# Kernel optimization log

Measured on AMD Instinct MI355X. Metric: run time of the kernel, lower is better.

Reference implementation:

```python
import jax, jax.numpy as jnp
import numpy as np

B, N, C, NH = 4, 2304, 256, 8
HD = C // NH            # head dim = 32
HS = WS = 48            # H = W = sqrt(N)
RADIUS = 3.0
MLP_HID = 4 * C
SCALE = HD ** (-0.5)
NEG = -1e9              # stands in for -inf (identical softmax up to fp eps)
EPS = 1e-6


def spatial_mask():
    # get_spatial_mask: cdist of (y, x) grid coords, -inf where dist > radius
    yy, xx = jnp.meshgrid(jnp.arange(HS), jnp.arange(WS), indexing='ij')
    coords = jnp.stack([yy, xx], -1).reshape(-1, 2).astype(jnp.float32)  # [N, 2]
    d2 = jnp.sum((coords[:, None, :] - coords[None, :, :]) ** 2, -1)     # [N, N]
    return jnp.where(d2 > RADIUS * RADIUS, NEG, 0.0)


def layernorm(x, g, b):
    mu = jnp.mean(x, -1, keepdims=True)
    var = jnp.mean((x - mu) ** 2, -1, keepdims=True)
    return (x - mu) * jax.lax.rsqrt(var + EPS) * g + b


def setup_inputs() -> dict:
    key = jax.random.key(0)
    ks = jax.random.split(key, 16)
    s = 0.02
    return {
        'x':    jax.random.normal(ks[0], (B, N, C), jnp.float32),
        'x_kv': jax.random.normal(ks[1], (B, N, C), jnp.float32),
        'Wq': jax.random.normal(ks[2], (C, C), jnp.float32) * s,
        'bq': jnp.zeros((C,), jnp.float32),
        'Wk': jax.random.normal(ks[3], (C, C), jnp.float32) * s,
        'bk': jnp.zeros((C,), jnp.float32),
        'Wv': jax.random.normal(ks[4], (C, C), jnp.float32) * s,
        'bv': jnp.zeros((C,), jnp.float32),
        'Wp': jax.random.normal(ks[5], (C, C), jnp.float32) * s,
        'bp': jnp.zeros((C,), jnp.float32),
        'g1': jnp.ones((C,), jnp.float32),
        'b1': jnp.zeros((C,), jnp.float32),
        'g2': jnp.ones((C,), jnp.float32),
        'b2': jnp.zeros((C,), jnp.float32),
        'W1': jax.random.normal(ks[6], (C, MLP_HID), jnp.float32) * s,
        'bm1': jnp.zeros((MLP_HID,), jnp.float32),
        'W2': jax.random.normal(ks[7], (MLP_HID, C), jnp.float32) * s,
        'bm2': jnp.zeros((C,), jnp.float32),
    }


def reference(x, x_kv, Wq, bq, Wk, bk, Wv, bv, Wp, bp,
              g1, b1, g2, b2, W1, bm1, W2, bm2):
    mask = spatial_mask()                                  # [N, N]
    h = layernorm(x, g1, b1)
    hkv = layernorm(x_kv, g1, b1)
    q = (h @ Wq + bq).reshape(B, N, NH, HD)
    k = (hkv @ Wk + bk).reshape(B, N, NH, HD)
    v = (hkv @ Wv + bv).reshape(B, N, NH, HD)
    scores = jnp.einsum('bqhd,bkhd->bhqk', q, k) * SCALE + mask
    attn = jax.nn.softmax(scores, axis=-1)
    out = jnp.einsum('bhqk,bkhd->bqhd', attn, v).reshape(B, N, C)
    x = x + out @ Wp + bp
    m = layernorm(x, g2, b2)
    x = x + jax.nn.gelu(m @ W1 + bm1, approximate=False) @ W2 + bm2
    return x
```

## Files before the change

kernel.cpp:

```cpp
#include <hip/hip_runtime.h>
#include <hip/hip_fp16.h>
#include <math.h>

#define BB 4
#define NN 2304
#define CC 256
#define HS 48
#define HID 1024
#define BNROWS (BB * NN)
#define ATTN_SCALE 0.17677669529663687f

typedef _Float16 f16;
typedef __attribute__((ext_vector_type(2))) _Float16 h2;
typedef __attribute__((ext_vector_type(8))) _Float16 h8;
typedef __attribute__((ext_vector_type(4))) float f4;

static __device__ __forceinline__ float wave_sum64(float v) {
    v += __shfl_xor(v, 32, 64);
    v += __shfl_xor(v, 16, 64);
    v += __shfl_xor(v, 8, 64);
    v += __shfl_xor(v, 4, 64);
    v += __shfl_xor(v, 2, 64);
    v += __shfl_xor(v, 1, 64);
    return v;
}

__global__ __launch_bounds__(256) void prep_kernel(
    const float* __restrict__ Wq, const float* __restrict__ Wk,
    const float* __restrict__ Wv, const float* __restrict__ Wp,
    const float* __restrict__ W1, const float* __restrict__ W2,
    const float* __restrict__ bq, const float* __restrict__ bk,
    const float* __restrict__ bv,
    f16* __restrict__ WqkvT, f16* __restrict__ WpT,
    f16* __restrict__ W1T, f16* __restrict__ W2T, float* __restrict__ bqkv)
{
    int bx = blockIdx.x;
    if (bx == 768) {
        const int t = threadIdx.x;
        bqkv[t]       = bq[t];
        bqkv[t + 256] = bk[t];
        bqkv[t + 512] = bv[t];
        return;
    }
    __shared__ float tt[32][33];
    const float* src; f16* dst; int K, N;
    if (bx < 64)        { src = Wq; dst = WqkvT;             K = 256;  N = 256; }
    else if (bx < 128)  { src = Wk; dst = WqkvT + 65536;     K = 256;  N = 256;  bx -= 64; }
    else if (bx < 192)  { src = Wv; dst = WqkvT + 131072;    K = 256;  N = 256;  bx -= 128; }
    else if (bx < 256)  { src = Wp; dst = WpT;               K = 256;  N = 256;  bx -= 192; }
    else if (bx < 512)  { src = W1; dst = W1T;               K = 256;  N = 1024; bx -= 256; }
    else                { src = W2; dst = W2T;               K = 1024; N = 256;  bx -= 512; }
    const int tN = N >> 5;
    const int kt = bx / tN, nt = bx - kt * tN;
    const int rr = threadIdx.x >> 5, cc = threadIdx.x & 31;
#pragma unroll
    for (int j = 0; j < 4; ++j)
        tt[rr + 8 * j][cc] = src[(size_t)(kt * 32 + rr + 8 * j) * N + nt * 32 + cc];
    __syncthreads();
#pragma unroll
    for (int j = 0; j < 4; ++j)
        dst[(size_t)(nt * 32 + rr + 8 * j) * K + kt * 32 + cc] = (f16)tt[cc][rr + 8 * j];
}

__global__ __launch_bounds__(256) void ln1_kernel(
    const float* __restrict__ x, const float* __restrict__ xkv,
    const float* __restrict__ g, const float* __restrict__ be,
    f16* __restrict__ hq, f16* __restrict__ hkv)
{
    const int r = blockIdx.x * 4 + (threadIdx.x >> 6);
    const int lane = threadIdx.x & 63;
    const float* src; f16* dst;
    if (r < BNROWS) { src = x + (size_t)r * CC;             dst = hq + (size_t)r * CC; }
    else { src = xkv + (size_t)(r - BNROWS) * CC; dst = hkv + (size_t)(r - BNROWS) * CC; }
    const float4 v = ((const float4*)src)[lane];
    const float mu = wave_sum64(v.x + v.y + v.z + v.w) * (1.0f / CC);
    const float d0 = v.x - mu, d1 = v.y - mu, d2 = v.z - mu, d3 = v.w - mu;
    const float var = wave_sum64(d0 * d0 + d1 * d1 + d2 * d2 + d3 * d3) * (1.0f / CC);
    const float rs = rsqrtf(var + 1e-6f);
    const float4 g4 = ((const float4*)g)[lane];
    const float4 b4 = ((const float4*)be)[lane];
    h2 o01 = (h2){(f16)(d0 * rs * g4.x + b4.x), (f16)(d1 * rs * g4.y + b4.y)};
    h2 o23 = (h2){(f16)(d2 * rs * g4.z + b4.z), (f16)(d3 * rs * g4.w + b4.w)};
    ((h2*)dst)[lane * 2] = o01;
    ((h2*)dst)[lane * 2 + 1] = o23;
}

__global__ __launch_bounds__(256) void ln2_kernel(
    const f16* __restrict__ x1, const float* __restrict__ g,
    const float* __restrict__ be, f16* __restrict__ m2)
{
    const int r = blockIdx.x * 4 + (threadIdx.x >> 6);
    const int lane = threadIdx.x & 63;
    const f16* src = x1 + (size_t)r * CC;
    const h2 a01 = ((const h2*)src)[lane * 2];
    const h2 a23 = ((const h2*)src)[lane * 2 + 1];
    const float v0 = (float)a01[0], v1 = (float)a01[1];
    const float v2 = (float)a23[0], v3 = (float)a23[1];
    const float mu = wave_sum64(v0 + v1 + v2 + v3) * (1.0f / CC);
    const float d0 = v0 - mu, d1 = v1 - mu, d2 = v2 - mu, d3 = v3 - mu;
    const float var = wave_sum64(d0 * d0 + d1 * d1 + d2 * d2 + d3 * d3) * (1.0f / CC);
    const float rs = rsqrtf(var + 1e-6f);
    const float4 g4 = ((const float4*)g)[lane];
    const float4 b4 = ((const float4*)be)[lane];
    f16* dst = m2 + (size_t)r * CC;
    h2 o01 = (h2){(f16)(d0 * rs * g4.x + b4.x), (f16)(d1 * rs * g4.y + b4.y)};
    h2 o23 = (h2){(f16)(d2 * rs * g4.z + b4.z), (f16)(d3 * rs * g4.w + b4.w)};
    ((h2*)dst)[lane * 2] = o01;
    ((h2*)dst)[lane * 2 + 1] = o23;
}

template <bool GELU, int RESID, bool OUTF32, bool QKV>
__global__ __launch_bounds__(256) void gemm64(
    const f16* __restrict__ Aq, const f16* __restrict__ Akv,
    const f16* __restrict__ Bt, const float* __restrict__ bias,
    const void* __restrict__ resid, void* __restrict__ out1,
    void* __restrict__ outkv, int M, int N, int K)
{
    __shared__ f16 As[64][72];
    __shared__ f16 Bs[64][72];
    const int tid = threadIdx.x;
    const int wid = tid >> 6, lane = tid & 63;
    const int ln15 = lane & 15, quad = lane >> 4;
    const int m0 = blockIdx.y * 64;
    const int n0 = blockIdx.x * 64;
    const bool kv = QKV && (n0 >= 256);
    const f16* Ap = (QKV && kv) ? Akv : Aq;

    const int sr = tid >> 2;
    const int sk = (tid & 3) << 4;

    f4 acc[4];
#pragma unroll
    for (int i = 0; i < 4; ++i) acc[i] = (f4){0.f, 0.f, 0.f, 0.f};

    for (int k0 = 0; k0 < K; k0 += 64) {
        const f16* ag = Ap + (size_t)(m0 + sr) * K + k0 + sk;
        const f16* bg = Bt + (size_t)(n0 + sr) * K + k0 + sk;
        *(uint4*)&As[sr][sk]     = *(const uint4*)ag;
        *(uint4*)&As[sr][sk + 8] = *(const uint4*)(ag + 8);
        *(uint4*)&Bs[sr][sk]     = *(const uint4*)bg;
        *(uint4*)&Bs[sr][sk + 8] = *(const uint4*)(bg + 8);
        __syncthreads();
#pragma unroll
        for (int kh = 0; kh < 2; ++kh) {
            const h8 bF = *(const h8*)&Bs[wid * 16 + ln15][kh * 32 + quad * 8];
#pragma unroll
            for (int mt = 0; mt < 4; ++mt) {
                const h8 aF = *(const h8*)&As[mt * 16 + ln15][kh * 32 + quad * 8];
                acc[mt] = __builtin_amdgcn_mfma_f32_16x16x32_f16(aF, bF, acc[mt], 0, 0, 0);
            }
        }
        __syncthreads();
    }

    const int gn = n0 + wid * 16 + ln15;
    const float bs = bias[gn];
#pragma unroll
    for (int mt = 0; mt < 4; ++mt) {
#pragma unroll
        for (int r = 0; r < 4; ++r) {
            const int gm = m0 + mt * 16 + quad * 4 + r;
            float v = acc[mt][r] + bs;
            if (GELU) v = 0.5f * v * (1.0f + erff(v * 0.70710678118654752f));
            if (RESID == 1) v += ((const float*)resid)[(size_t)gm * N + gn];
            if (RESID == 2) v += (float)((const f16*)resid)[(size_t)gm * N + gn];
            if (QKV) {
                if (kv) ((f16*)outkv)[(size_t)gm * 512 + (gn - 256)] = (f16)v;
                else    ((f16*)out1)[(size_t)gm * 256 + gn] = (f16)v;
            } else if (OUTF32) {
                ((float*)out1)[(size_t)gm * N + gn] = v;
            } else {
                ((f16*)out1)[(size_t)gm * N + gn] = (f16)v;
            }
        }
    }
}

__device__ __constant__ int ATT_DY[29] = {
    -3, -2, -2, -2, -2, -2, -1, -1, -1, -1, -1, 0, 0, 0, 0,
    0, 0, 0, 1, 1, 1, 1, 1, 2, 2, 2, 2, 2, 3};
__device__ __constant__ int ATT_DX[29] = {
    0, -2, -1, 0, 1, 2, -2, -1, 0, 1, 2, -3, -2, -1, 0,
    1, 2, 3, -2, -1, 0, 1, 2, -2, -1, 0, 1, 2, 0};

__global__ __launch_bounds__(128) void attn_tile_kernel(
    const f16* __restrict__ qf, const f16* __restrict__ kvf,
    f16* __restrict__ ao)
{
    __shared__ f16 ks[196][66];
    __shared__ f16 vs[196][66];
    const int tile = blockIdx.x, hp = blockIdx.y, b = blockIdx.z;
    const int ty0 = (tile / 6) * 8, tx0 = (tile - (tile / 6) * 6) * 8;
    const int tid = threadIdx.x;

    for (int idx = tid; idx < 196 * 16; idx += 128) {
        const int r = idx >> 4, seg = idx & 15;
        const int gy = ty0 - 3 + r / 14, gx = tx0 - 3 + (r - (r / 14) * 14);
        uint4 val = {0u, 0u, 0u, 0u};
        if ((unsigned)gy < HS && (unsigned)gx < HS) {
            const size_t rowb = ((size_t)b * NN + gy * HS + gx) * 512;
            const int ch = (seg < 8) ? (hp * 64 + seg * 8)
                                     : (256 + hp * 64 + (seg - 8) * 8);
            val = *(const uint4*)&kvf[rowb + ch];
        }
        f16* dstp = (seg < 8) ? &ks[r][(seg & 7) * 8] : &vs[r][(seg & 7) * 8];
        ((unsigned int*)dstp)[0] = val.x;
        ((unsigned int*)dstp)[1] = val.y;
        ((unsigned int*)dstp)[2] = val.z;
        ((unsigned int*)dstp)[3] = val.w;
    }
    __syncthreads();

    const int q = tid & 63, hh = tid >> 6;
    const int qy = q >> 3, qx = q & 7;
    const size_t qrow = (size_t)b * NN + (ty0 + qy) * HS + tx0 + qx;
    const f16* qp = qf + qrow * CC + hp * 64 + hh * 32;
    uint4 qa[4];
#pragma unroll
    for (int i = 0; i < 4; ++i) qa[i] = ((const uint4*)qp)[i];
    const h2* q2 = (const h2*)qa;

    float s[29];
#pragma unroll
    for (int n = 0; n < 29; ++n) {
        const int dy = ATT_DY[n], dx = ATT_DX[n];
        const int r = (qy + 3 + dy) * 14 + qx + 3 + dx;
        const bool valid = (unsigned)(ty0 + qy + dy) < HS &&
                           (unsigned)(tx0 + qx + dx) < HS;
        float a = 0.0f;
        const h2* kp = (const h2*)&ks[r][hh * 32];
#pragma unroll
        for (int i = 0; i < 16; ++i)
            a = __builtin_amdgcn_fdot2(q2[i], kp[i], a, false);
        s[n] = valid ? a * ATTN_SCALE : -1e30f;
    }
    float m = s[0];
#pragma unroll
    for (int n = 1; n < 29; ++n) m = fmaxf(m, s[n]);
    float l = 0.0f;
#pragma unroll
    for (int n = 0; n < 29; ++n) { s[n] = __expf(s[n] - m); l += s[n]; }
    h2 a2[16];
#pragma unroll
    for (int i = 0; i < 16; ++i) a2[i] = (h2){(f16)0.f, (f16)0.f};
#pragma unroll
    for (int n = 0; n < 29; ++n) {
        const int dy = ATT_DY[n], dx = ATT_DX[n];
        const int r = (qy + 3 + dy) * 14 + qx + 3 + dx;
        const f16 pn = (f16)s[n];
        const h2 ph = (h2){pn, pn};
        const h2* vp = (const h2*)&vs[r][hh * 32];
#pragma unroll
        for (int i = 0; i < 16; ++i) a2[i] += ph * vp[i];
    }
    const float inv = 1.0f / l;
    uint4 ov[4];
    f16* oh = (f16*)ov;
#pragma unroll
    for (int i = 0; i < 16; ++i) {
        oh[2 * i]     = (f16)((float)a2[i][0] * inv);
        oh[2 * i + 1] = (f16)((float)a2[i][1] * inv);
    }
    uint4* dst = (uint4*)(ao + qrow * CC + hp * 64 + hh * 32);
#pragma unroll
    for (int i = 0; i < 4; ++i) dst[i] = ov[i];
}

extern "C" void kernel_launch(void* const* d_in, const int* in_sizes, int n_in,
                              void* d_out, int out_size, void* d_ws, size_t ws_size,
                              hipStream_t stream) {
    const float* x    = (const float*)d_in[0];
    const float* x_kv = (const float*)d_in[1];
    const float* Wq   = (const float*)d_in[2];
    const float* bq   = (const float*)d_in[3];
    const float* Wk   = (const float*)d_in[4];
    const float* bk   = (const float*)d_in[5];
    const float* Wv   = (const float*)d_in[6];
    const float* bv   = (const float*)d_in[7];
    const float* Wp   = (const float*)d_in[8];
    const float* bp   = (const float*)d_in[9];
    const float* g1   = (const float*)d_in[10];
    const float* b1   = (const float*)d_in[11];
    const float* g2   = (const float*)d_in[12];
    const float* b2   = (const float*)d_in[13];
    const float* W1   = (const float*)d_in[14];
    const float* bm1  = (const float*)d_in[15];
    const float* W2   = (const float*)d_in[16];
    const float* bm2  = (const float*)d_in[17];
    float* outp = (float*)d_out;

    f16* wsh = (f16*)d_ws;
    f16* WqkvT = wsh;
    f16* WpT   = wsh + 196608;
    f16* W1T   = wsh + 262144;
    f16* W2T   = wsh + 524288;
    float* bqkv = (float*)(wsh + 786432);
    f16* hq    = wsh + 787968;
    f16* hkv   = wsh + 3147264;
    f16* qf    = wsh + 5506560;
    f16* kvf   = wsh + 7865856;
    f16* ao    = hq;
    f16* x1    = hkv;
    f16* m2    = qf;
    f16* hidF  = kvf;
    const bool fused = ws_size >= (size_t)17303040 * sizeof(f16);

    prep_kernel<<<769, 256, 0, stream>>>(Wq, Wk, Wv, Wp, W1, W2, bq, bk, bv,
                                         WqkvT, WpT, W1T, W2T, bqkv);
    ln1_kernel<<<2 * BNROWS / 4, 256, 0, stream>>>(x, x_kv, g1, b1, hq, hkv);
    gemm64<false, 0, false, true><<<dim3(12, 144), 256, 0, stream>>>(
        hq, hkv, WqkvT, bqkv, nullptr, qf, kvf, BNROWS, 768, CC);
    attn_tile_kernel<<<dim3(36, 4, BB), 128, 0, stream>>>(qf, kvf, ao);
    gemm64<false, 1, false, false><<<dim3(4, 144), 256, 0, stream>>>(
        ao, nullptr, WpT, bp, x, x1, nullptr, BNROWS, CC, CC);
    ln2_kernel<<<BNROWS / 4, 256, 0, stream>>>(x1, g2, b2, m2);
    if (fused) {
        gemm64<true, 0, false, false><<<dim3(16, 144), 256, 0, stream>>>(
            m2, nullptr, W1T, bm1, nullptr, hidF, nullptr, BNROWS, HID, CC);
        gemm64<false, 2, true, false><<<dim3(4, 144), 256, 0, stream>>>(
            hidF, nullptr, W2T, bm2, x1, outp, nullptr, BNROWS, CC, HID);
    } else {
        for (int b = 0; b < BB; ++b) {
            const size_t off = (size_t)b * NN * CC;
            gemm64<true, 0, false, false><<<dim3(16, 36), 256, 0, stream>>>(
                m2 + off, nullptr, W1T, bm1, nullptr, hidF, nullptr, NN, HID, CC);
            gemm64<false, 2, true, false><<<dim3(4, 36), 256, 0, stream>>>(
                hidF, nullptr, W2T, bm2, x1 + off, outp + off, nullptr, NN, CC, HID);
        }
    }
    (void)in_sizes; (void)n_in; (void)out_size;
}
```

Measured before the change: 200.1 us.

## Rewrite GEMMs as per-wave tiles using direct global-to-LDS loads with swizzle

Replaces the block-cooperative 64x64 GEMM with a kernel where each wave owns its own TM x 64 output tile and private LDS staging, so no block-wide barriers are needed. Tiles are loaded with global_load_lds (direct global-to-LDS DMA) into an XOR-style swizzled layout to avoid bank conflicts, and each wave now computes AT x 4 MFMA tiles per K step, raising register-level reuse of A and B fragments. Grid sizes are shrunk to match the larger per-block M coverage. The loads are not double-buffered, so each K step waits on its own global loads, and per-wave tiles mean B is fetched redundantly by each wave.

After: 196.9 us. About the same (-1.6%).

```diff
diff --git a/kernel.cpp b/kernel.cpp
--- a/kernel.cpp
+++ b/kernel.cpp
@@ -14,6 +14,14 @@
 typedef __attribute__((ext_vector_type(2))) _Float16 h2;
 typedef __attribute__((ext_vector_type(8))) _Float16 h8;
 typedef __attribute__((ext_vector_type(4))) float f4;
+
+#define GLLS16(g, l)                                                        \
+    __builtin_amdgcn_global_load_lds(                                       \
+        (const __attribute__((address_space(1))) unsigned int*)(g),         \
+        (__attribute__((address_space(3))) unsigned int*)(l), 16, 0, 0)
+
+#define WAIT_VM0()   asm volatile("s_waitcnt vmcnt(0)" ::: "memory")
+#define WAIT_LGKM0() asm volatile("s_waitcnt lgkmcnt(0)" ::: "memory")
 
 static __device__ __forceinline__ float wave_sum64(float v) {
     v += __shfl_xor(v, 32, 64);
@@ -109,68 +117,102 @@
     ((h2*)dst)[lane * 2 + 1] = o23;
 }
 
-template <bool GELU, int RESID, bool OUTF32, bool QKV>
-__global__ __launch_bounds__(256) void gemm64(
+template <int TM, bool GELU, int RESID, bool OUTF32, bool QKV>
+__global__ __launch_bounds__(256, 4) void gemm_wave(
     const f16* __restrict__ Aq, const f16* __restrict__ Akv,
     const f16* __restrict__ Bt, const float* __restrict__ bias,
     const void* __restrict__ resid, void* __restrict__ out1,
     void* __restrict__ outkv, int M, int N, int K)
 {
-    __shared__ f16 As[64][72];
-    __shared__ f16 Bs[64][72];
+    constexpr int AT = TM / 16;
+    constexpr int AELEM = TM * 32;
+    __shared__ f16 lds[4 * (AELEM + 2048)];
     const int tid = threadIdx.x;
     const int wid = tid >> 6, lane = tid & 63;
     const int ln15 = lane & 15, quad = lane >> 4;
-    const int m0 = blockIdx.y * 64;
+    f16* Al = lds + wid * (AELEM + 2048);
+    f16* Bl = Al + AELEM;
     const int n0 = blockIdx.x * 64;
-    const bool kv = QKV && (n0 >= 256);
-    const f16* Ap = (QKV && kv) ? Akv : Aq;
-
-    const int sr = tid >> 2;
-    const int sk = (tid & 3) << 4;
-
-    f4 acc[4];
-#pragma unroll
-    for (int i = 0; i < 4; ++i) acc[i] = (f4){0.f, 0.f, 0.f, 0.f};
-
-    for (int k0 = 0; k0 < K; k0 += 64) {
-        const f16* ag = Ap + (size_t)(m0 + sr) * K + k0 + sk;
-        const f16* bg = Bt + (size_t)(n0 + sr) * K + k0 + sk;
-        *(uint4*)&As[sr][sk]     = *(const uint4*)ag;
-        *(uint4*)&As[sr][sk + 8] = *(const uint4*)(ag + 8);
-        *(uint4*)&Bs[sr][sk]     = *(const uint4*)bg;
-        *(uint4*)&Bs[sr][sk + 8] = *(const uint4*)(bg + 8);
-        __syncthreads();
-#pragma unroll
-        for (int kh = 0; kh < 2; ++kh) {
-            const h8 bF = *(const h8*)&Bs[wid * 16 + ln15][kh * 32 + quad * 8];
-#pragma unroll
-            for (int mt = 0; mt < 4; ++mt) {
-                const h8 aF = *(const h8*)&As[mt * 16 + ln15][kh * 32 + quad * 8];
-                acc[mt] = __builtin_amdgcn_mfma_f32_16x16x32_f16(aF, bF, acc[mt], 0, 0, 0);
-            }
-        }
-        __syncthreads();
-    }
-
-    const int gn = n0 + wid * 16 + ln15;
-    const float bs = bias[gn];
-#pragma unroll
-    for (int mt = 0; mt < 4; ++mt) {
-#pragma unroll
-        for (int r = 0; r < 4; ++r) {
-            const int gm = m0 + mt * 16 + quad * 4 + r;
-            float v = acc[mt][r] + bs;
-            if (GELU) v = 0.5f * v * (1.0f + erff(v * 0.70710678118654752f));
-            if (RESID == 1) v += ((const float*)resid)[(size_t)gm * N + gn];
-            if (RESID == 2) v += (float)((const f16*)resid)[(size_t)gm * N + gn];
-            if (QKV) {
-                if (kv) ((f16*)outkv)[(size_t)gm * 512 + (gn - 256)] = (f16)v;
-                else    ((f16*)out1)[(size_t)gm * 256 + gn] = (f16)v;
-            } else if (OUTF32) {
-                ((float*)out1)[(size_t)gm * N + gn] = v;
-            } else {
-                ((f16*)out1)[(size_t)gm * N + gn] = (f16)v;
+    const int m0 = (blockIdx.y * 4 + wid) * TM;
+    const f16* Ap = QKV ? (n0 < 256 ? Aq : Akv) : Aq;
+
+    const int jr = lane >> 2, js = lane & 3;
+    size_t ga[AT], gb[4];
+#pragma unroll
+    for (int i = 0; i < AT; ++i) {
+        const int r = i * 16 + jr;
+        const int q = (js - (r >> 1)) & 3;
+        ga[i] = (size_t)(m0 + r) * K + q * 8;
+    }
+#pragma unroll
+    for (int i = 0; i < 4; ++i) {
+        const int r = i * 16 + jr;
+        const int q = (js - (r >> 1)) & 3;
+        gb[i] = (size_t)(n0 + r) * K + q * 8;
+    }
+    int aoff[AT], boff[4];
+#pragma unroll
+    for (int mt = 0; mt < AT; ++mt) {
+        const int r = mt * 16 + ln15;
+        aoff[mt] = (r * 4 + ((quad + (r >> 1)) & 3)) * 16;
+    }
+#pragma unroll
+    for (int nt = 0; nt < 4; ++nt) {
+        const int r = nt * 16 + ln15;
+        boff[nt] = (r * 4 + ((quad + (r >> 1)) & 3)) * 16;
+    }
+
+    f4 acc[AT][4];
+#pragma unroll
+    for (int i = 0; i < AT; ++i)
+#pragma unroll
+        for (int j = 0; j < 4; ++j) acc[i][j] = (f4){0.f, 0.f, 0.f, 0.f};
+
+    for (int k0 = 0; k0 < K; k0 += 32) {
+        if (k0) WAIT_LGKM0();
+#pragma unroll
+        for (int i = 0; i < AT; ++i)
+            GLLS16(Ap + ga[i] + k0, Al + i * 512);
+#pragma unroll
+        for (int i = 0; i < 4; ++i)
+            GLLS16(Bt + gb[i] + k0, Bl + i * 512);
+        WAIT_VM0();
+        h8 bF[4], aF[AT];
+#pragma unroll
+        for (int nt = 0; nt < 4; ++nt)
+            bF[nt] = *(const h8*)((const char*)Bl + boff[nt]);
+#pragma unroll
+        for (int mt = 0; mt < AT; ++mt)
+            aF[mt] = *(const h8*)((const char*)Al + aoff[mt]);
+#pragma unroll
+        for (int mt = 0; mt < AT; ++mt)
+#pragma unroll
+            for (int nt = 0; nt < 4; ++nt)
+                acc[mt][nt] = __builtin_amdgcn_mfma_f32_16x16x32_f16(
+                    aF[mt], bF[nt], acc[mt][nt], 0, 0, 0);
+    }
+
+#pragma unroll
+    for (int nt = 0; nt < 4; ++nt) {
+        const int gn = n0 + nt * 16 + ln15;
+        const float bs = bias[gn];
+#pragma unroll
+        for (int mt = 0; mt < AT; ++mt) {
+#pragma unroll
+            for (int r = 0; r < 4; ++r) {
+                const int gm = m0 + mt * 16 + quad * 4 + r;
+                float v = acc[mt][nt][r] + bs;
+                if (GELU) v = 0.5f * v * (1.0f + erff(v * 0.70710678118654752f));
+                if (RESID == 1) v += ((const float*)resid)[(size_t)gm * N + gn];
+                if (RESID == 2) v += (float)((const f16*)resid)[(size_t)gm * N + gn];
+                if (QKV) {
+                    if (gn < 256) ((f16*)out1)[(size_t)gm * 256 + gn] = (f16)v;
+                    else ((f16*)outkv)[(size_t)gm * 512 + (gn - 256)] = (f16)v;
+                } else if (OUTF32) {
+                    ((float*)out1)[(size_t)gm * N + gn] = v;
+                } else {
+                    ((f16*)out1)[(size_t)gm * N + gn] = (f16)v;
+                }
             }
         }
     }
@@ -308,23 +350,23 @@
     prep_kernel<<<769, 256, 0, stream>>>(Wq, Wk, Wv, Wp, W1, W2, bq, bk, bv,
                                          WqkvT, WpT, W1T, W2T, bqkv);
     ln1_kernel<<<2 * BNROWS / 4, 256, 0, stream>>>(x, x_kv, g1, b1, hq, hkv);
-    gemm64<false, 0, false, true><<<dim3(12, 144), 256, 0, stream>>>(
+    gemm_wave<64, false, 0, false, true><<<dim3(12, 36), 256, 0, stream>>>(
         hq, hkv, WqkvT, bqkv, nullptr, qf, kvf, BNROWS, 768, CC);
     attn_tile_kernel<<<dim3(36, 4, BB), 128, 0, stream>>>(qf, kvf, ao);
-    gemm64<false, 1, false, false><<<dim3(4, 144), 256, 0, stream>>>(
+    gemm_wave<32, false, 1, false, false><<<dim3(4, 72), 256, 0, stream>>>(
         ao, nullptr, WpT, bp, x, x1, nullptr, BNROWS, CC, CC);
     ln2_kernel<<<BNROWS / 4, 256, 0, stream>>>(x1, g2, b2, m2);
     if (fused) {
-        gemm64<true, 0, false, false><<<dim3(16, 144), 256, 0, stream>>>(
+        gemm_wave<64, true, 0, false, false><<<dim3(16, 36), 256, 0, stream>>>(
             m2, nullptr, W1T, bm1, nullptr, hidF, nullptr, BNROWS, HID, CC);
-        gemm64<false, 2, true, false><<<dim3(4, 144), 256, 0, stream>>>(
+        gemm_wave<32, false, 2, true, false><<<dim3(4, 72), 256, 0, stream>>>(
             hidF, nullptr, W2T, bm2, x1, outp, nullptr, BNROWS, CC, HID);
     } else {
         for (int b = 0; b < BB; ++b) {
             const size_t off = (size_t)b * NN * CC;
-            gemm64<true, 0, false, false><<<dim3(16, 36), 256, 0, stream>>>(
+            gemm_wave<64, true, 0, false, false><<<dim3(16, 9), 256, 0, stream>>>(
                 m2 + off, nullptr, W1T, bm1, nullptr, hidF, nullptr, NN, HID, CC);
-            gemm64<false, 2, true, false><<<dim3(4, 36), 256, 0, stream>>>(
+            gemm_wave<32, false, 2, true, false><<<dim3(4, 18), 256, 0, stream>>>(
                 hidF, nullptr, W2T, bm2, x1 + off, outp + off, nullptr, NN, CC, HID);
         }
     }
```
